# Kernel optimization log

Hardware: AMD Instinct MI355X
Metric: run time of the kernel (lower is better)

Reference implementation:

```python
import jax, jax.numpy as jnp
import numpy as np

B, C, T = 8, 64, 128

def _conv(x, w, b, stride=1, pad=1, groups=1):
    y = jax.lax.conv_general_dilated(x, w, (stride, stride), [(pad, pad), (pad, pad)],
                                     feature_group_count=groups,
                                     dimension_numbers=('NCHW', 'OIHW', 'NCHW'))
    return y + b[None, :, None, None]

def _lrelu(x):
    return jnp.where(x > 0, x, 0.1 * x)

def _ps4(A, Bt, Ct, Dt):
    # qiancha(A,B,C,D) interleaves channels with stride 4; PixelShuffle(2) then maps
    # group index j in [0..3] to pixel offset (j//2, j%2): A->(0,0), B->(0,1), C->(1,0), D->(1,1)
    b, c, h, w = A.shape
    s = jnp.stack([A, Bt, Ct, Dt], axis=2).reshape(b, c, 2, 2, h, w)
    return s.transpose(0, 1, 4, 2, 5, 3).reshape(b, c, 2 * h, 2 * w)

def _il2(A, Bt):
    # qiancha2: stride-2 channel interleave
    b, c, h, w = A.shape
    return jnp.stack([A, Bt], axis=2).reshape(b, 2 * c, h, w)

def setup_inputs():
    key = jax.random.key(0)
    ks = jax.random.split(key, 20)
    def w(k, shape):
        return 0.05 * jax.random.normal(k, shape, dtype=jnp.float32)
    d = {}
    d['x'] = jax.random.normal(ks[0], (B, C, T, T), dtype=jnp.float32)
    d['w_hwc'] = w(ks[1], (3 * C, C, 1, 1)); d['b_hwc'] = w(ks[2], (3 * C,))
    d['w_dw'] = w(ks[3], (3 * C, 1, 3, 3)); d['b_dw'] = w(ks[4], (3 * C,))
    d['w_hw'] = w(ks[5], (C, C, 3, 3)); d['b_hw'] = w(ks[6], (C,))
    d['w_cw'] = w(ks[7], (T, T, 3, 3)); d['b_cw'] = w(ks[8], (T,))
    d['w_hc'] = w(ks[9], (T, T, 3, 3)); d['b_hc'] = w(ks[10], (T,))
    d['w_down'] = w(ks[11], (C, 2 * C, 2, 2)); d['b_down'] = w(ks[12], (C,))
    d['w_l1'] = w(ks[13], (C, C, 3, 3)); d['b_l1'] = w(ks[14], (C,))
    d['w_l2'] = w(ks[15], (C, C, 3, 3)); d['b_l2'] = w(ks[16], (C,))
    return d

def reference(x, w_hwc, b_hwc, w_dw, b_dw, w_hw, b_hw, w_cw, b_cw, w_hc, b_hc,
              w_down, b_down, w_l1, b_l1, w_l2, b_l2):
    c = x.shape[1]
    # 1x1 expand then depthwise 3x3 -> three gating maps
    hwc = _conv(_conv(x, w_hwc, b_hwc, pad=0), w_dw, b_dw, pad=1, groups=3 * c)
    HW, CW, HC = jnp.split(hwc, 3, axis=1)
    x_hw = _lrelu(_conv(x, w_hw, b_hw)) * HW
    x_cw = _lrelu(_conv(x.transpose(0, 2, 1, 3), w_cw, b_cw)).transpose(0, 2, 1, 3) * CW
    x_hc = _lrelu(_conv(x.transpose(0, 3, 2, 1), w_hc, b_hc)).transpose(0, 3, 2, 1) * HC
    xqc1 = _ps4(x, x_hw, x_cw, x_hc)
    xqc2 = _ps4(x_hc, x_cw, x_hw, x)
    xqc = _il2(xqc1, xqc2)                              # [B, 2C, 2T, 2T]
    out = _conv(xqc, w_down, b_down, stride=2, pad=0) + x
    out1 = _lrelu(_conv(out, w_l1, b_l1))
    out1 = _lrelu(_conv(out1, w_l2, b_l2))
    return x + out1
```

## Files before the change

### kernel.cpp

```cpp
#include <hip/hip_runtime.h>
#include <hip/hip_bf16.h>

#define BB 8
#define CC 64
#define TT 128
#define PP (TT*TT)
#define C3 192

typedef __hip_bfloat16 bf16;
typedef __attribute__((ext_vector_type(8))) short short8;
typedef __attribute__((ext_vector_type(4))) float floatx4;

__device__ __forceinline__ float b2f(bf16 v){ return __bfloat162float(v); }
__device__ __forceinline__ bf16 f2b(float v){ return __float2bfloat16(v); }
__device__ __forceinline__ short8 lds8(const bf16* p){ return *(const short8*)(const void*)p; }

__global__ void k_wpk(const float* __restrict__ w_down, const float* __restrict__ w_hc,
                      const float* __restrict__ w_cw,  const float* __restrict__ w_hwc,
                      const float* __restrict__ w_hw,  const float* __restrict__ w_l1,
                      const float* __restrict__ w_l2,  const float* __restrict__ w_dw,
                      const float* __restrict__ b_hwc, const float* __restrict__ b_dw,
                      bf16* __restrict__ wpkd,
                      bf16* __restrict__ wpkhw, bf16* __restrict__ wpkl1,
                      bf16* __restrict__ wpkl2, bf16* __restrict__ wpkcw,
                      bf16* __restrict__ wpkhc, bf16* __restrict__ wpkgm,
                      float* __restrict__ bg){
  int i = blockIdx.x*256 + threadIdx.x;
  if (i < 147456){
    int j = i & 7, lane = (i>>3) & 63, mm = (i>>9) & 7, kk = (i>>12) & 3, t = i >> 14;
    int m = mm*16 + (lane & 15);
    int k = kk*32 + (lane>>4)*8 + j;
    wpkcw[i] = f2b(w_cw[m*1152 + k*9 + t]);
    wpkhc[i] = f2b(w_hc[m*1152 + k*9 + t]);
  }
  if (i < 147456){
    int j = i & 7, lane = (i>>3) & 63, s = (i>>9) & 3;
    int rest = i >> 11;
    int t2k = rest % 18, wv = rest / 18;
    int t = t2k >> 1, kk = t2k & 1;
    int lm = lane & 15;
    int ic = kk*32 + (lane>>4)*8 + j;
    float val;
    if (s == 0){
      val = w_hw[(wv*16 + lm)*576 + ic*9 + t];
    } else {
      int grp = (s == 1) ? wv : (s == 2) ? 4 + wv : 8 + wv;
      int oc = grp*16 + lm;
      val = w_dw[oc*9 + t] * w_hwc[oc*64 + ic];
    }
    wpkgm[i] = f2b(val);
  }
  if (i < 36864){
    int j = i & 7, lane = (i>>3) & 63, mm = (i>>9) & 3, kk = (i>>11) & 1, t = i >> 12;
    int oc = mm*16 + (lane & 15);
    int ic = kk*32 + (lane>>4)*8 + j;
    int s = oc*576 + ic*9 + t;
    wpkhw[i] = f2b(w_hw[s]);
    wpkl1[i] = f2b(w_l1[s]);
    wpkl2[i] = f2b(w_l2[s]);
  }
  if (i < 1728){
    int cls = i / C3, oc = i % C3;
    int ch = cls / 3, cw = cls % 3;
    float S = 0.f;
    for (int dh = (ch==0?1:0); dh <= (ch==2?1:2); ++dh)
      for (int dw = (cw==0?1:0); dw <= (cw==2?1:2); ++dw)
        S += w_dw[oc*9 + dh*3 + dw];
    bg[cls*C3 + oc] = b_dw[oc] + b_hwc[oc]*S;
  }
  if (i < 16384){
    int j = i & 7, lane = (i>>3) & 63, mm = (i>>9) & 3, kk = i >> 11;
    int m = mm*16 + (lane & 15);
    int k = kk*32 + (lane>>4)*8 + j;
    int s = k >> 6, c = k & 63;
    wpkd[i] = f2b(w_down[m*512 + c*8 + s] + w_down[m*512 + c*8 + 7 - s]);
  }
}

__global__ void k_pack(const float* __restrict__ x, bf16* __restrict__ xh,
                       bf16* __restrict__ xb16){
  int h = blockIdx.x, b = blockIdx.y;
  __shared__ float xs[64][129];
  for (int idx = threadIdx.x; idx < 2048; idx += 256){
    int c = idx >> 5, w4 = (idx & 31)*4;
    float4 v = *(const float4*)(x + ((size_t)b*CC + c)*PP + h*TT + w4);
    bf16 o4[4] = { f2b(v.x), f2b(v.y), f2b(v.z), f2b(v.w) };
    *(uint2*)(xb16 + ((size_t)b*CC + c)*PP + h*TT + w4) = *(uint2*)o4;
    xs[c][w4] = v.x; xs[c][w4+1] = v.y; xs[c][w4+2] = v.z; xs[c][w4+3] = v.w;
  }
  __syncthreads();
  for (int idx = threadIdx.x; idx < 8192; idx += 256){
    int w = idx >> 6, c = idx & 63;
    xh[(((size_t)b*TT + h)*TT + w)*64 + c] = f2b(xs[c][w]);
  }
}

__global__ void k_xw(const bf16* __restrict__ xb16, bf16* __restrict__ xW){
  int c = blockIdx.x, b = blockIdx.y;
  __shared__ unsigned short xs2[32][140];
  const bf16* src = xb16 + ((size_t)b*CC + c)*PP;
  unsigned short* dst = (unsigned short*)(xW + ((size_t)b*CC + c)*PP);
  for (int s = 0; s < 4; ++s){
    if (s) __syncthreads();
    for (int idx = threadIdx.x; idx < 512; idx += 256){
      int hl = idx >> 4, w8 = (idx & 15)*8;
      unsigned short tmp[8];
      *(uint4*)tmp = *(const uint4*)(src + (s*32 + hl)*TT + w8);
      #pragma unroll
      for (int j = 0; j < 8; ++j) xs2[hl][w8+j] = tmp[j];
    }
    __syncthreads();
    for (int idx = threadIdx.x; idx < 4096; idx += 256){
      int w = idx >> 5, hl = idx & 31;
      dst[w*TT + s*32 + hl] = xs2[hl][w];
    }
  }
}

__global__ __launch_bounds__(256)
void k_ghwm(const bf16* __restrict__ xh, const bf16* __restrict__ wpkgm,
            const float* __restrict__ bg,
            const float* __restrict__ b_hw, bf16* __restrict__ xhwh,
            bf16* __restrict__ g, int NB){
  int L = blockIdx.x;
  int b = L % NB; int r0 = L / NB;
  int h = r0 % TT; int w0b = (r0 / TT)*64;
  int tid = threadIdx.x, lane = tid & 63, wv = tid >> 6;
  int nlo = lane & 15, quad = lane >> 4;
  __shared__ bf16 xs[3][66][64];
  for (int idx = tid; idx < 1584; idx += 256){
    int dh = idx / 528, rr = idx % 528, wi = rr >> 3, ch = rr & 7;
    int gh = h + dh - 1, gw = w0b + wi - 1;
    uint4 v = make_uint4(0,0,0,0);
    if (gh >= 0 && gh < TT && gw >= 0 && gw < TT)
      v = *(const uint4*)(xh + (((size_t)b*TT + gh)*TT + gw)*64 + ch*8);
    *(uint4*)(&xs[dh][wi][((ch ^ (wi & 7)))*8]) = v;
  }
  __syncthreads();
  const bf16* pa = wpkgm + (size_t)wv*36864 + lane*8;
  floatx4 acc[4][4] = {};
  #pragma unroll
  for (int t = 0; t < 9; ++t){
    int dh = t/3, dw = t%3;
    int swk = (nlo + dw) & 7;
    #pragma unroll
    for (int kk = 0; kk < 2; ++kk){
      int pc = ((kk*4 + quad) ^ swk)*8;
      short8 bfv[4];
      #pragma unroll
      for (int nn = 0; nn < 4; ++nn)
        bfv[nn] = lds8(&xs[dh][nn*16 + nlo + dw][pc]);
      const bf16* base = pa + (t*2 + kk)*2048;
      short8 a0 = *(const short8*)(const void*)(base);
      short8 a1 = *(const short8*)(const void*)(base + 512);
      short8 a2 = *(const short8*)(const void*)(base + 1024);
      short8 a3 = *(const short8*)(const void*)(base + 1536);
      #pragma unroll
      for (int nn = 0; nn < 4; ++nn){
        acc[0][nn] = __builtin_amdgcn_mfma_f32_16x16x32_bf16(a0, bfv[nn], acc[0][nn], 0,0,0);
        acc[1][nn] = __builtin_amdgcn_mfma_f32_16x16x32_bf16(a1, bfv[nn], acc[1][nn], 0,0,0);
        acc[2][nn] = __builtin_amdgcn_mfma_f32_16x16x32_bf16(a2, bfv[nn], acc[2][nn], 0,0,0);
        acc[3][nn] = __builtin_amdgcn_mfma_f32_16x16x32_bf16(a3, bfv[nn], acc[3][nn], 0,0,0);
      }
    }
  }
  int ch_cls3 = ((h == 0) ? 0 : (h == TT-1) ? 2 : 1)*3;
  int oc0 = wv*16 + quad*4;
  float4 bhw = *(const float4*)(b_hw + oc0);
  #pragma unroll
  for (int nn = 0; nn < 4; ++nn){
    int w = w0b + nn*16 + nlo;
    int cw_cls = (w == 0) ? 0 : (w == TT-1) ? 2 : 1;
    const float* bgrow = bg + (ch_cls3 + cw_cls)*C3;
    float4 bg0 = *(const float4*)(bgrow + oc0);
    float bga[4] = { bg0.x, bg0.y, bg0.z, bg0.w };
    float bha[4] = { bhw.x, bhw.y, bhw.z, bhw.w };
    bf16 o4[4];
    #pragma unroll
    for (int r = 0; r < 4; ++r){
      float hv = acc[0][nn][r] + bha[r];
      hv = hv > 0.f ? hv : 0.1f*hv;
      float gv = b2f(f2b(acc[1][nn][r] + bga[r]));
      o4[r] = f2b(hv * gv);
    }
    *(uint2*)(xhwh + (((size_t)b*PP + h*TT + w))*64 + oc0) = *(uint2*)o4;
  }
  __syncthreads();
  bf16* tb = &xs[0][0][0];
  #pragma unroll
  for (int p = 0; p < 2; ++p){
    #pragma unroll
    for (int nn = 0; nn < 4; ++nn){
      int wl = nn*16 + nlo;
      int w = w0b + wl;
      int cw_cls = (w == 0) ? 0 : (w == TT-1) ? 2 : 1;
      float4 bgp = *(const float4*)(bg + (ch_cls3 + cw_cls)*C3 + 64 + p*64 + oc0);
      float bga[4] = { bgp.x, bgp.y, bgp.z, bgp.w };
      #pragma unroll
      for (int r = 0; r < 4; ++r)
        tb[(p*64 + oc0 + r)*72 + wl] = f2b(acc[2+p][nn][r] + bga[r]);
    }
  }
  __syncthreads();
  #pragma unroll
  for (int i = 0; i < 4; ++i){
    int idx = i*256 + tid;
    int row = idx >> 3, wc = (idx & 7)*8;
    uint4 v = *(const uint4*)(tb + row*72 + wc);
    *(uint4*)(g + ((size_t)b*C3 + 64 + row)*PP + h*TT + w0b + wc) = v;
  }
}

__global__ __launch_bounds__(256)
void k_c3x3m(const bf16* __restrict__ in, const bf16* __restrict__ wpk,
             const float* __restrict__ bias,
             const float* __restrict__ resx, bf16* __restrict__ yb,
             float* __restrict__ yf, int mode, int NB){
  int L = blockIdx.x;
  int b = L % NB, h = L / NB;
  int tid = threadIdx.x, lane = tid & 63, wv = tid >> 6;
  int nlo = lane & 15, quad = lane >> 4;
  __shared__ bf16 xs[3][130][64];
  for (int idx = tid; idx < 3120; idx += 256){
    int dh = idx / 1040, r = idx % 1040, wi = r >> 3, ch = r & 7;
    int gh = h + dh - 1, gw = wi - 1;
    uint4 v = make_uint4(0,0,0,0);
    if (gh >= 0 && gh < TT && gw >= 0 && gw < TT)
      v = *(const uint4*)(in + (((size_t)b*TT + gh)*TT + gw)*64 + ch*8);
    *(uint4*)(&xs[dh][wi][((ch ^ (wi & 7)))*8]) = v;
  }
  __syncthreads();
  floatx4 acc[8] = {};
  #pragma unroll
  for (int t = 0; t < 9; ++t){
    int dh = t/3, dw = t%3;
    int swk = (nlo + dw) & 7;
    #pragma unroll
    for (int kk = 0; kk < 2; ++kk){
      short8 a = *(const short8*)(const void*)(wpk + (((t*2+kk)*4+wv)*64 + lane)*8);
      int pc = ((kk*4 + quad) ^ swk)*8;
      #pragma unroll
      for (int nn = 0; nn < 8; ++nn){
        short8 bf = lds8(&xs[dh][nn*16 + nlo + dw][pc]);
        acc[nn] = __builtin_amdgcn_mfma_f32_16x16x32_bf16(a, bf, acc[nn], 0,0,0);
      }
    }
  }
  int oc0 = wv*16 + quad*4;
  float4 bs = *(const float4*)(bias + oc0);
  float bsa[4] = { bs.x, bs.y, bs.z, bs.w };
  #pragma unroll
  for (int nn = 0; nn < 8; ++nn){
    int w = nn*16 + nlo;
    int pi = h*TT + w;
    if (mode == 1){
      bf16 o4[4];
      #pragma unroll
      for (int r = 0; r < 4; ++r){
        float v = acc[nn][r] + bsa[r];
        o4[r] = f2b(v > 0.f ? v : 0.1f*v);
      }
      *(uint2*)(yb + ((size_t)b*PP + pi)*64 + oc0) = *(uint2*)o4;
    } else {
      #pragma unroll
      for (int r = 0; r < 4; ++r){
        int oc = oc0 + r;
        float v = acc[nn][r] + bsa[r];
        v = v > 0.f ? v : 0.1f*v;
        yf[((size_t)b*CC + oc)*PP + pi] = v + resx[((size_t)b*CC + oc)*PP + pi];
      }
    }
  }
}

__global__ __launch_bounds__(256)
void k_cwm(const bf16* __restrict__ xW, const bf16* __restrict__ wpkcw,
           const float* __restrict__ bias, const bf16* __restrict__ g,
           bf16* __restrict__ xcw, int NB){
  int L = blockIdx.x;
  int b = L % NB; int r0 = L / NB;
  int c = r0 % CC; int w0b = (r0 / CC)*64;
  int tid = threadIdx.x, lane = tid & 63, wv = tid >> 6;
  int nlo = lane & 15, quad = lane >> 4;
  __shared__ bf16 xs[66][128];
  floatx4 acc[2][4] = {};
  for (int dc = 0; dc < 3; ++dc){
    int cc = c + dc - 1;
    if (cc < 0 || cc >= CC) continue;
    __syncthreads();
    for (int idx = tid; idx < 1056; idx += 256){
      int s = idx >> 4, ch = idx & 15;
      int gw = w0b - 1 + s;
      uint4 v = make_uint4(0,0,0,0);
      if (gw >= 0 && gw < TT)
        v = *(const uint4*)(xW + (((size_t)b*CC + cc)*TT + gw)*TT + ch*8);
      *(uint4*)(&xs[s][((ch ^ (s & 7)))*8]) = v;
    }
    __syncthreads();
    #pragma unroll
    for (int dw = 0; dw < 3; ++dw){
      int t = dc*3 + dw;
      int swk = (nlo + dw) & 7;
      #pragma unroll
      for (int kk = 0; kk < 4; ++kk){
        short8 a0 = *(const short8*)(const void*)(wpkcw + (((t*4+kk)*8 + wv*2    )*64 + lane)*8);
        short8 a1 = *(const short8*)(const void*)(wpkcw + (((t*4+kk)*8 + wv*2 + 1)*64 + lane)*8);
        int pc = ((kk*4 + quad) ^ swk)*8;
        #pragma unroll
        for (int nn = 0; nn < 4; ++nn){
          short8 bf = lds8(&xs[nn*16 + nlo + dw][pc]);
          acc[0][nn] = __builtin_amdgcn_mfma_f32_16x16x32_bf16(a0, bf, acc[0][nn], 0,0,0);
          acc[1][nn] = __builtin_amdgcn_mfma_f32_16x16x32_bf16(a1, bf, acc[1][nn], 0,0,0);
        }
      }
    }
  }
  #pragma unroll
  for (int ml = 0; ml < 2; ++ml){
    int ho0 = (wv*2 + ml)*16 + quad*4;
    float4 bs = *(const float4*)(bias + ho0);
    float bsa[4] = { bs.x, bs.y, bs.z, bs.w };
    #pragma unroll
    for (int nn = 0; nn < 4; ++nn){
      int w = w0b + nn*16 + nlo;
      #pragma unroll
      for (int r = 0; r < 4; ++r){
        int ho = ho0 + r;
        float v = acc[ml][nn][r] + bsa[r];
        v = v > 0.f ? v : 0.1f*v;
        v *= b2f(g[((size_t)b*C3 + 64 + c)*PP + ho*TT + w]);
        xcw[((size_t)b*CC + c)*PP + ho*TT + w] = f2b(v);
      }
    }
  }
}

__global__ __launch_bounds__(256)
void k_hcm(const bf16* __restrict__ xb16, const bf16* __restrict__ wpkhc,
           const float* __restrict__ bias, const bf16* __restrict__ g,
           bf16* __restrict__ xhch, int NB){
  int L = blockIdx.x;
  int b = L % NB, h = L / NB;
  int tid = threadIdx.x, lane = tid & 63, wv = tid >> 6;
  int nlo = lane & 15, quad = lane >> 4;
  __shared__ bf16 xs[66][128];
  floatx4 acc[2][4] = {};
  for (int dh = 0; dh < 3; ++dh){
    int gh = h + dh - 1;
    __syncthreads();
    for (int idx = tid; idx < 1056; idx += 256){
      int s = idx >> 4, ch = idx & 15;
      int cc = s - 1;
      uint4 v = make_uint4(0,0,0,0);
      if (cc >= 0 && cc < CC && gh >= 0 && gh < TT)
        v = *(const uint4*)(xb16 + (((size_t)b*CC + cc)*TT + gh)*TT + ch*8);
      *(uint4*)(&xs[s][((ch ^ (s & 7)))*8]) = v;
    }
    __syncthreads();
    #pragma unroll
    for (int dc = 0; dc < 3; ++dc){
      int t = dh*3 + dc;
      int swk = (nlo + dc) & 7;
      #pragma unroll
      for (int kk = 0; kk < 4; ++kk){
        short8 a0 = *(const short8*)(const void*)(wpkhc + (((t*4+kk)*8 + wv*2    )*64 + lane)*8);
        short8 a1 = *(const short8*)(const void*)(wpkhc + (((t*4+kk)*8 + wv*2 + 1)*64 + lane)*8);
        int pc = ((kk*4 + quad) ^ swk)*8;
        #pragma unroll
        for (int nn = 0; nn < 4; ++nn){
          short8 bf = lds8(&xs[nn*16 + nlo + dc][pc]);
          acc[0][nn] = __builtin_amdgcn_mfma_f32_16x16x32_bf16(a0, bf, acc[0][nn], 0,0,0);
          acc[1][nn] = __builtin_amdgcn_mfma_f32_16x16x32_bf16(a1, bf, acc[1][nn], 0,0,0);
        }
      }
    }
  }
  #pragma unroll
  for (int ml = 0; ml < 2; ++ml){
    int wo0 = (wv*2 + ml)*16 + quad*4;
    float4 bs = *(const float4*)(bias + wo0);
    float bsa[4] = { bs.x, bs.y, bs.z, bs.w };
    #pragma unroll
    for (int nn = 0; nn < 4; ++nn){
      int c = nn*16 + nlo;
      bf16 gg[4];
      *(uint2*)gg = *(const uint2*)(g + ((size_t)b*C3 + 128 + c)*PP + h*TT + wo0);
      #pragma unroll
      for (int r = 0; r < 4; ++r){
        float v = acc[ml][nn][r] + bsa[r];
        v = v > 0.f ? v : 0.1f*v;
        xhch[((size_t)b*PP + h*TT + wo0 + r)*64 + c] = f2b(v * b2f(gg[r]));
      }
    }
  }
}

__global__ __launch_bounds__(256)
void k_downm(const bf16* __restrict__ xh, const bf16* __restrict__ xhwh,
             const bf16* __restrict__ xcwn, const bf16* __restrict__ xhch,
             const bf16* __restrict__ wpkd, const float* __restrict__ x,
             const float* __restrict__ bias, bf16* __restrict__ outh){
  int h = blockIdx.x, b = blockIdx.y;
  int tid = threadIdx.x, lane = tid & 63, wv = tid >> 6;
  int nlo = lane & 15, quad = lane >> 4;
  int p0 = h*TT;
  __shared__ bf16 xs[128][76];
  for (int idx = tid; idx < 1024; idx += 256){
    int c = idx >> 4, w8 = (idx & 15)*8;
    bf16 tmp[8];
    *(uint4*)tmp = *(const uint4*)(xcwn + ((size_t)b*CC + c)*PP + p0 + w8);
    #pragma unroll
    for (int j = 0; j < 8; ++j) xs[w8+j][c] = tmp[j];
  }
  __syncthreads();
  int n0 = wv*32;
  floatx4 acc[4][2] = {};
  #pragma unroll
  for (int kk = 0; kk < 8; ++kk){
    int s = kk >> 1;
    int ko = (kk & 1)*32 + quad*8;
    short8 bfr[2];
    #pragma unroll
    for (int nn = 0; nn < 2; ++nn){
      int p = n0 + nn*16 + nlo;
      if (s == 2){
        bfr[nn] = lds8(&xs[p][ko]);
      } else {
        const bf16* src = (s == 0) ? xh : (s == 1) ? xhwh : xhch;
        bfr[nn] = *(const short8*)(const void*)(src + ((size_t)b*PP + p0 + p)*64 + ko);
      }
    }
    #pragma unroll
    for (int mm = 0; mm < 4; ++mm){
      short8 a = *(const short8*)(const void*)(wpkd + ((kk*4+mm)*64 + lane)*8);
      acc[mm][0] = __builtin_amdgcn_mfma_f32_16x16x32_bf16(a, bfr[0], acc[mm][0], 0,0,0);
      acc[mm][1] = __builtin_amdgcn_mfma_f32_16x16x32_bf16(a, bfr[1], acc[mm][1], 0,0,0);
    }
  }
  #pragma unroll
  for (int mm = 0; mm < 4; ++mm){
    int o0 = mm*16 + quad*4;
    float4 bs = *(const float4*)(bias + o0);
    float bsa[4] = { bs.x, bs.y, bs.z, bs.w };
    #pragma unroll
    for (int nn = 0; nn < 2; ++nn){
      int p = n0 + nn*16 + nlo;
      bf16 o4[4];
      #pragma unroll
      for (int r = 0; r < 4; ++r){
        float v = acc[mm][nn][r] + bsa[r] + x[((size_t)b*CC + o0 + r)*PP + p0 + p];
        o4[r] = f2b(v);
      }
      *(uint2*)(outh + ((size_t)b*PP + p0 + p)*64 + o0) = *(uint2*)o4;
    }
  }
}

extern "C" void kernel_launch(void* const* d_in, const int* in_sizes, int n_in,
                              void* d_out, int out_size, void* d_ws, size_t ws_size,
                              hipStream_t stream) {
  const float* x      = (const float*)d_in[0];
  const float* w_hwc  = (const float*)d_in[1];
  const float* b_hwc  = (const float*)d_in[2];
  const float* w_dw   = (const float*)d_in[3];
  const float* b_dw   = (const float*)d_in[4];
  const float* w_hw   = (const float*)d_in[5];
  const float* b_hw   = (const float*)d_in[6];
  const float* w_cw   = (const float*)d_in[7];
  const float* b_cw   = (const float*)d_in[8];
  const float* w_hc   = (const float*)d_in[9];
  const float* b_hc   = (const float*)d_in[10];
  const float* w_down = (const float*)d_in[11];
  const float* b_down = (const float*)d_in[12];
  const float* w_l1   = (const float*)d_in[13];
  const float* b_l1   = (const float*)d_in[14];
  const float* w_l2   = (const float*)d_in[15];
  const float* b_l2   = (const float*)d_in[16];
  float* out = (float*)d_out;

  char* ws = (char*)d_ws;
  bf16*  wpkd  = (bf16*) (ws + 0);
  float* bg    = (float*)(ws + 36864);
  bf16*  wpkhw = (bf16*) (ws + 65536);
  bf16*  wpkl1 = (bf16*) (ws + 139264);
  bf16*  wpkl2 = (bf16*) (ws + 212992);
  bf16*  wpkcw = (bf16*) (ws + 294912);
  bf16*  wpkhc = (bf16*) (ws + 589824);
  bf16*  wpkgm = (bf16*) (ws + 884736);

  k_wpk<<<576, 256, 0, stream>>>(w_down, w_hc, w_cw, w_hwc, w_hw, w_l1, w_l2,
                                 w_dw, b_hwc, b_dw,
                                 wpkd, wpkhw, wpkl1, wpkl2, wpkcw, wpkhc,
                                 wpkgm, bg);

  if (ws_size >= 153092096ull) {
    bf16* g    = (bf16*)(ws + 2097152);
    bf16* xh   = (bf16*)(ws + 52428800);
    bf16* xW   = (bf16*)(ws + 69206016);
    bf16* xb16 = (bf16*)(ws + 85983232);
    bf16* xhwh = (bf16*)(ws + 102760448);
    bf16* xcw  = (bf16*)(ws + 119537664);
    bf16* xhch = (bf16*)(ws + 136314880);
    bf16* outh = xW;
    bf16* o1h  = xb16;

    k_pack<<<dim3(TT, BB), 256, 0, stream>>>(x, xh, xb16);
    k_xw<<<dim3(CC, BB), 256, 0, stream>>>(xb16, xW);
    k_ghwm<<<2*TT*BB, 256, 0, stream>>>(xh, wpkgm, bg, b_hw, xhwh, g, BB);
    k_cwm  <<<2*CC*BB, 256, 0, stream>>>(xW, wpkcw, b_cw, g, xcw, BB);
    k_hcm  <<<TT*BB, 256, 0, stream>>>(xb16, wpkhc, b_hc, g, xhch, BB);
    k_downm<<<dim3(TT, BB), 256, 0, stream>>>(xh, xhwh, xcw, xhch, wpkd, x, b_down, outh);
    k_c3x3m<<<TT*BB, 256, 0, stream>>>(outh, wpkl1, b_l1, nullptr, o1h, nullptr, 1, BB);
    k_c3x3m<<<TT*BB, 256, 0, stream>>>(o1h, wpkl2, b_l2, x, nullptr, out, 2, BB);
  } else {
    char* P = ws + 2097152;
    bf16* g_b    = (bf16*)(P);
    bf16* xh_b   = (bf16*)(P + 6291456);
    bf16* xW_b   = (bf16*)(P + 8388608);
    bf16* xb_b   = (bf16*)(P + 10485760);
    bf16* xhwh_b = (bf16*)(P + 12582912);
    bf16* xcw_b  = (bf16*)(P + 14680064);
    bf16* xhch_b = (bf16*)(P + 16777216);
    bf16* outh_b = xW_b;
    bf16* o1h_b  = xb_b;
    for (int b = 0; b < BB; ++b){
      const float* xb = x + (size_t)b*CC*PP;
      float* outb = out + (size_t)b*CC*PP;
      k_pack<<<dim3(TT, 1), 256, 0, stream>>>(xb, xh_b, xb_b);
      k_xw<<<dim3(CC, 1), 256, 0, stream>>>(xb_b, xW_b);
      k_ghwm<<<2*TT, 256, 0, stream>>>(xh_b, wpkgm, bg, b_hw, xhwh_b, g_b, 1);
      k_cwm  <<<2*CC, 256, 0, stream>>>(xW_b, wpkcw, b_cw, g_b, xcw_b, 1);
      k_hcm  <<<TT, 256, 0, stream>>>(xb_b, wpkhc, b_hc, g_b, xhch_b, 1);
      k_downm<<<dim3(TT, 1), 256, 0, stream>>>(xh_b, xhwh_b, xcw_b, xhch_b, wpkd, xb, b_down, outh_b);
      k_c3x3m<<<TT, 256, 0, stream>>>(outh_b, wpkl1, b_l1, nullptr, o1h_b, nullptr, 1, 1);
      k_c3x3m<<<TT, 256, 0, stream>>>(o1h_b, wpkl2, b_l2, xb, nullptr, outb, 2, 1);
    }
  }
}
```

Before: 285.8 us.

## Fuse HC-branch conv into down-projection kernel via shared-memory tile

Merges the HC-axis 3x3 conv kernel with the 2x2 down-projection kernel. Each block keeps its HC gated result for one row in LDS instead of writing it to global memory and reading it back in a separate launch. This removes a kernel launch and the global round trip of the xhch tensor. In exchange it uses more LDS per block (about 38 KB), which may lower occupancy. The fused kernel also changes the block index mapping to b = L % NB, which alters the tile scheduling order relative to the old down kernel.

```diff
diff --git a/kernel.cpp b/kernel.cpp
--- a/kernel.cpp
+++ b/kernel.cpp
@@ -336,14 +336,20 @@
 }
 
 __global__ __launch_bounds__(256)
-void k_hcm(const bf16* __restrict__ xb16, const bf16* __restrict__ wpkhc,
-           const float* __restrict__ bias, const bf16* __restrict__ g,
-           bf16* __restrict__ xhch, int NB){
+void k_hcdm(const bf16* __restrict__ xb16, const bf16* __restrict__ wpkhc,
+            const float* __restrict__ b_hc, const bf16* __restrict__ g,
+            const bf16* __restrict__ xh, const bf16* __restrict__ xhwh,
+            const bf16* __restrict__ xcwn, const bf16* __restrict__ wpkd,
+            const float* __restrict__ x, const float* __restrict__ b_down,
+            bf16* __restrict__ outh, int NB){
   int L = blockIdx.x;
   int b = L % NB, h = L / NB;
   int tid = threadIdx.x, lane = tid & 63, wv = tid >> 6;
   int nlo = lane & 15, quad = lane >> 4;
-  __shared__ bf16 xs[66][128];
+  __shared__ bf16 shm[9728 + 9216];
+  bf16* bufC = shm;
+  bf16* tb   = shm + 9728;
+  bf16 (*xs)[128] = (bf16(*)[128])bufC;
   floatx4 acc[2][4] = {};
   for (int dh = 0; dh < 3; ++dh){
     int gh = h + dh - 1;
@@ -378,7 +384,7 @@
   #pragma unroll
   for (int ml = 0; ml < 2; ++ml){
     int wo0 = (wv*2 + ml)*16 + quad*4;
-    float4 bs = *(const float4*)(bias + wo0);
+    float4 bs = *(const float4*)(b_hc + wo0);
     float bsa[4] = { bs.x, bs.y, bs.z, bs.w };
     #pragma unroll
     for (int nn = 0; nn < 4; ++nn){
@@ -389,32 +395,22 @@
       for (int r = 0; r < 4; ++r){
         float v = acc[ml][nn][r] + bsa[r];
         v = v > 0.f ? v : 0.1f*v;
-        xhch[((size_t)b*PP + h*TT + wo0 + r)*64 + c] = f2b(v * b2f(gg[r]));
-      }
-    }
-  }
-}
-
-__global__ __launch_bounds__(256)
-void k_downm(const bf16* __restrict__ xh, const bf16* __restrict__ xhwh,
-             const bf16* __restrict__ xcwn, const bf16* __restrict__ xhch,
-             const bf16* __restrict__ wpkd, const float* __restrict__ x,
-             const float* __restrict__ bias, bf16* __restrict__ outh){
-  int h = blockIdx.x, b = blockIdx.y;
-  int tid = threadIdx.x, lane = tid & 63, wv = tid >> 6;
-  int nlo = lane & 15, quad = lane >> 4;
+        tb[(wo0 + r)*72 + c] = f2b(v * b2f(gg[r]));
+      }
+    }
+  }
+  __syncthreads();
   int p0 = h*TT;
-  __shared__ bf16 xs[128][76];
   for (int idx = tid; idx < 1024; idx += 256){
     int c = idx >> 4, w8 = (idx & 15)*8;
     bf16 tmp[8];
     *(uint4*)tmp = *(const uint4*)(xcwn + ((size_t)b*CC + c)*PP + p0 + w8);
     #pragma unroll
-    for (int j = 0; j < 8; ++j) xs[w8+j][c] = tmp[j];
+    for (int j = 0; j < 8; ++j) bufC[(w8+j)*76 + c] = tmp[j];
   }
   __syncthreads();
   int n0 = wv*32;
-  floatx4 acc[4][2] = {};
+  floatx4 acc2[4][2] = {};
   #pragma unroll
   for (int kk = 0; kk < 8; ++kk){
     int s = kk >> 1;
@@ -424,23 +420,25 @@
     for (int nn = 0; nn < 2; ++nn){
       int p = n0 + nn*16 + nlo;
       if (s == 2){
-        bfr[nn] = lds8(&xs[p][ko]);
+        bfr[nn] = lds8(&bufC[p*76 + ko]);
+      } else if (s == 3){
+        bfr[nn] = lds8(&tb[p*72 + ko]);
       } else {
-        const bf16* src = (s == 0) ? xh : (s == 1) ? xhwh : xhch;
+        const bf16* src = (s == 0) ? xh : xhwh;
         bfr[nn] = *(const short8*)(const void*)(src + ((size_t)b*PP + p0 + p)*64 + ko);
       }
     }
     #pragma unroll
     for (int mm = 0; mm < 4; ++mm){
       short8 a = *(const short8*)(const void*)(wpkd + ((kk*4+mm)*64 + lane)*8);
-      acc[mm][0] = __builtin_amdgcn_mfma_f32_16x16x32_bf16(a, bfr[0], acc[mm][0], 0,0,0);
-      acc[mm][1] = __builtin_amdgcn_mfma_f32_16x16x32_bf16(a, bfr[1], acc[mm][1], 0,0,0);
+      acc2[mm][0] = __builtin_amdgcn_mfma_f32_16x16x32_bf16(a, bfr[0], acc2[mm][0], 0,0,0);
+      acc2[mm][1] = __builtin_amdgcn_mfma_f32_16x16x32_bf16(a, bfr[1], acc2[mm][1], 0,0,0);
     }
   }
   #pragma unroll
   for (int mm = 0; mm < 4; ++mm){
     int o0 = mm*16 + quad*4;
-    float4 bs = *(const float4*)(bias + o0);
+    float4 bs = *(const float4*)(b_down + o0);
     float bsa[4] = { bs.x, bs.y, bs.z, bs.w };
     #pragma unroll
     for (int nn = 0; nn < 2; ++nn){
@@ -448,7 +446,7 @@
       bf16 o4[4];
       #pragma unroll
       for (int r = 0; r < 4; ++r){
-        float v = acc[mm][nn][r] + bsa[r] + x[((size_t)b*CC + o0 + r)*PP + p0 + p];
+        float v = acc2[mm][nn][r] + bsa[r] + x[((size_t)b*CC + o0 + r)*PP + p0 + p];
         o4[r] = f2b(v);
       }
       *(uint2*)(outh + ((size_t)b*PP + p0 + p)*64 + o0) = *(uint2*)o4;
@@ -500,7 +498,6 @@
     bf16* xb16 = (bf16*)(ws + 85983232);
     bf16* xhwh = (bf16*)(ws + 102760448);
     bf16* xcw  = (bf16*)(ws + 119537664);
-    bf16* xhch = (bf16*)(ws + 136314880);
     bf16* outh = xW;
     bf16* o1h  = xb16;
 
@@ -508,8 +505,8 @@
     k_xw<<<dim3(CC, BB), 256, 0, stream>>>(xb16, xW);
     k_ghwm<<<2*TT*BB, 256, 0, stream>>>(xh, wpkgm, bg, b_hw, xhwh, g, BB);
     k_cwm  <<<2*CC*BB, 256, 0, stream>>>(xW, wpkcw, b_cw, g, xcw, BB);
-    k_hcm  <<<TT*BB, 256, 0, stream>>>(xb16, wpkhc, b_hc, g, xhch, BB);
-    k_downm<<<dim3(TT, BB), 256, 0, stream>>>(xh, xhwh, xcw, xhch, wpkd, x, b_down, outh);
+    k_hcdm<<<TT*BB, 256, 0, stream>>>(xb16, wpkhc, b_hc, g, xh, xhwh, xcw,
+                                      wpkd, x, b_down, outh, BB);
     k_c3x3m<<<TT*BB, 256, 0, stream>>>(outh, wpkl1, b_l1, nullptr, o1h, nullptr, 1, BB);
     k_c3x3m<<<TT*BB, 256, 0, stream>>>(o1h, wpkl2, b_l2, x, nullptr, out, 2, BB);
   } else {
@@ -520,7 +517,6 @@
     bf16* xb_b   = (bf16*)(P + 10485760);
     bf16* xhwh_b = (bf16*)(P + 12582912);
     bf16* xcw_b  = (bf16*)(P + 14680064);
-    bf16* xhch_b = (bf16*)(P + 16777216);
     bf16* outh_b = xW_b;
     bf16* o1h_b  = xb_b;
     for (int b = 0; b < BB; ++b){
@@ -530,8 +526,8 @@
       k_xw<<<dim3(CC, 1), 256, 0, stream>>>(xb_b, xW_b);
       k_ghwm<<<2*TT, 256, 0, stream>>>(xh_b, wpkgm, bg, b_hw, xhwh_b, g_b, 1);
       k_cwm  <<<2*CC, 256, 0, stream>>>(xW_b, wpkcw, b_cw, g_b, xcw_b, 1);
-      k_hcm  <<<TT, 256, 0, stream>>>(xb_b, wpkhc, b_hc, g_b, xhch_b, 1);
-      k_downm<<<dim3(TT, 1), 256, 0, stream>>>(xh_b, xhwh_b, xcw_b, xhch_b, wpkd, xb, b_down, outh_b);
+      k_hcdm<<<TT, 256, 0, stream>>>(xb_b, wpkhc, b_hc, g_b, xh_b, xhwh_b, xcw_b,
+                                     wpkd, xb, b_down, outh_b, 1);
       k_c3x3m<<<TT, 256, 0, stream>>>(outh_b, wpkl1, b_l1, nullptr, o1h_b, nullptr, 1, 1);
       k_c3x3m<<<TT, 256, 0, stream>>>(o1h_b, wpkl2, b_l2, xb, nullptr, outb, 2, 1);
     }
```

Result: slower. 291.6 us, median of 3 (+2.0%).
